# Performance work log

Measured on AMD Instinct MI355X. Metric: run time of the kernel, lower is better.

The kernel has to match this reference:

```python
import jax, jax.numpy as jnp
import numpy as np

N = 4096
IN_DIM = 256
HID = 64
NHEADS = 4
OUT_DIM = 128
ALPHA = 0.5  # LeakyReLU negative slope
NEG_INF = -9e15


def gat_layer(x, mask, W, a, concat):
    """Dense GraphAttentionLayer (pyGAT style).
    x:[N,Fin], mask:[N,N] bool, W:[Fin,Fout], a:[2*Fout]."""
    Wh = x @ W                                   # [N, Fout]
    Fout = W.shape[1]
    f1 = Wh @ a[:Fout]                           # [N]
    f2 = Wh @ a[Fout:]                           # [N]
    e = jax.nn.leaky_relu(f1[:, None] + f2[None, :], negative_slope=ALPHA)  # [N,N]
    att = jax.nn.softmax(jnp.where(mask, e, NEG_INF), axis=1)               # [N,N]
    h = att @ Wh                                 # [N, Fout]
    return jax.nn.elu(h) if concat else h


def setup_inputs() -> dict:
    key = jax.random.key(0)
    ks = jax.random.split(key, 6)
    x = jax.random.normal(ks[0], (N, IN_DIM), dtype=jnp.float32)
    adj = jax.random.randint(ks[1], (N, N), 0, 2, dtype=jnp.int32)
    s_in = 1.0 / np.sqrt(IN_DIM)
    s_hid = 1.0 / np.sqrt(HID * NHEADS)
    W_heads = jax.random.uniform(ks[2], (NHEADS, IN_DIM, HID), jnp.float32, -s_in, s_in)
    a_heads = jax.random.uniform(ks[3], (NHEADS, 2 * HID), jnp.float32, -s_in, s_in)
    W_out = jax.random.uniform(ks[4], (HID * NHEADS, OUT_DIM), jnp.float32, -s_hid, s_hid)
    a_out = jax.random.uniform(ks[5], (2 * OUT_DIM,), jnp.float32, -s_hid, s_hid)
    return {"x": x, "adj": adj, "W_heads": W_heads, "a_heads": a_heads,
            "W_out": W_out, "a_out": a_out}


def reference(x, adj, W_heads, a_heads, W_out, a_out):
    mask = adj > 0
    # multi-head attention, concat along feature dim
    heads = jax.vmap(lambda W, a: gat_layer(x, mask, W, a, True))(W_heads, a_heads)
    h = jnp.transpose(heads, (1, 0, 2)).reshape(N, NHEADS * HID)  # [N, H*HID]
    # dropout=0 -> identity; final GAT layer (concat=False) + outer ELU
    out = jax.nn.elu(gat_layer(h, mask, W_out, a_out, False))     # [N, OUT_DIM]
    return out
```

## Files before the change

kernel.cpp:

```cpp
#include <hip/hip_runtime.h>
#include <hip/hip_bf16.h>

#define N 4096
#define IN_DIM 256
#define HID 64
#define NHEADS 4
#define OUT_DIM 128
#define LOG2E 1.44269504088896340736f

typedef __attribute__((ext_vector_type(8))) short bf16x8;
typedef __attribute__((ext_vector_type(4))) float f32x4;

__global__ __launch_bounds__(256, 4) void prep_kernel(
        const float* __restrict__ x, const float* __restrict__ W,
        const float* __restrict__ a, const int* __restrict__ adj,
        __hip_bfloat16* __restrict__ WhB,
        float* __restrict__ f1, float* __restrict__ f2,
        unsigned* __restrict__ maskT) {
    __shared__ float xs[8 * IN_DIM];
    const int t = threadIdx.x;
    if (blockIdx.x < 512) {
        const int c = t & 63, h = t >> 6;
        const int i0 = blockIdx.x * 8;
        const float4* xg = (const float4*)(x + (size_t)i0 * IN_DIM);
        float4* xs4 = (float4*)xs;
        for (int u = t; u < 8 * IN_DIM / 4; u += 256) xs4[u] = xg[u];
        __syncthreads();
        float acc[8];
#pragma unroll
        for (int r = 0; r < 8; r++) acc[r] = 0.f;
        const float* Wp = W + (size_t)h * IN_DIM * HID + c;
        for (int k = 0; k < IN_DIM; k += 4) {
            const float w0 = Wp[(size_t)(k + 0) * HID];
            const float w1 = Wp[(size_t)(k + 1) * HID];
            const float w2 = Wp[(size_t)(k + 2) * HID];
            const float w3 = Wp[(size_t)(k + 3) * HID];
#pragma unroll
            for (int r = 0; r < 8; r++) {
                const float4 xv = *(const float4*)(xs + r * IN_DIM + k);
                acc[r] += xv.x * w0 + xv.y * w1 + xv.z * w2 + xv.w * w3;
            }
        }
        union { ushort u[8]; uint4 v; } cv;
#pragma unroll
        for (int r = 0; r < 8; r++)
            cv.u[r] = __hip_bfloat16_raw(__float2bfloat16(acc[r])).x;
        const int jblk = i0 >> 5, quad = (i0 >> 3) & 3;
        const int lane_idx = (c & 15) + 16 * quad;
        *(uint4*)(WhB + ((((size_t)h * (N / 32) + jblk) * 4 + (c >> 4)) * 64 +
                         lane_idx) * 8) = cv.v;
        const float av1 = a[h * 2 * HID + c];
        const float av2 = a[h * 2 * HID + HID + c];
        float s1[8], s2[8];
#pragma unroll
        for (int r = 0; r < 8; r++) { s1[r] = acc[r] * av1; s2[r] = acc[r] * av2; }
#pragma unroll
        for (int mm = 32; mm > 0; mm >>= 1) {
#pragma unroll
            for (int r = 0; r < 8; r++) {
                s1[r] += __shfl_xor(s1[r], mm, 64);
                s2[r] += __shfl_xor(s2[r], mm, 64);
            }
        }
        if (c == 0) {
#pragma unroll
            for (int r = 0; r < 8; r++) {
                f1[(size_t)h * N + i0 + r] = s1[r] * LOG2E;
                f2[(size_t)h * N + i0 + r] = s2[r] * LOG2E;
            }
        }
    } else {
        const int lane = t & 63, w = t >> 6;
        const int i = (blockIdx.x - 512) * 4 + w;
        const int4* arow = (const int4*)(adj + (size_t)i * N);
        for (int jb = 0; jb < N / 256; jb++) {
            const int4 a4 = arow[jb * 64 + lane];
            unsigned long long bal[4];
            bal[0] = __ballot(a4.x > 0);
            bal[1] = __ballot(a4.y > 0);
            bal[2] = __ballot(a4.z > 0);
            bal[3] = __ballot(a4.w > 0);
            if (lane < 8) {
                unsigned word = 0;
#pragma unroll
                for (int e = 0; e < 4; e++) {
                    unsigned xv = (unsigned)(bal[e] >> (8 * lane)) & 0xFFu;
                    xv = (xv | (xv << 12)) & 0x000F000Fu;
                    xv = (xv | (xv << 6))  & 0x03030303u;
                    xv = (xv | (xv << 3))  & 0x11111111u;
                    word |= xv << e;
                }
                maskT[(size_t)(jb * 8 + lane) * N + i] = word;
            }
        }
    }
}

template <int HEADS, int D, int DSL, int G, int MW>
__global__ __launch_bounds__(G * 64, 4) void attn_fused(
        const unsigned* __restrict__ maskT,
        const __hip_bfloat16* __restrict__ WhB,
        const float* __restrict__ f1g, const float* __restrict__ f2g,
        float* __restrict__ outp) {
    constexpr int CTtot = D / 16;
    constexpr int CTT = CTtot / DSL;
    constexpr int CC = (D == 64) ? 1 : 2;
    constexpr int KSTEPS = N / (32 * G);
    __shared__ float sh[MW * G * 16 * CC * 17];
    __shared__ float dsh[MW * G * 16];
    const int t = threadIdx.x;
    const int g = t >> 6, lane = t & 63;
    const int m = lane & 15, quad = lane >> 4;
    const int h = blockIdx.y / DSL, slc = blockIdx.y % DSL;
    const int i0 = blockIdx.x * (16 * MW);

    float f1v[MW];
#pragma unroll
    for (int mw = 0; mw < MW; mw++)
        f1v[mw] = f1g[(size_t)h * N + i0 + mw * 16 + m];
    const float* f2p = f2g + (size_t)h * N;
    const bf16x8* whb = (const bf16x8*)WhB + (size_t)h * (N / 32) * CTtot * 64;

    const f32x4 zero = {0.f, 0.f, 0.f, 0.f};
    f32x4 acc[MW][CTT];
    f32x4 sac[MW];
#pragma unroll
    for (int mw = 0; mw < MW; mw++) {
        sac[mw] = zero;
#pragma unroll
        for (int ct = 0; ct < CTT; ct++) acc[mw][ct] = zero;
    }
    const short one_bf = (short)0x3F80;
    const bf16x8 ones = {one_bf, one_bf, one_bf, one_bf,
                         one_bf, one_bf, one_bf, one_bf};

    unsigned mwrd[2][MW];
    float f2v[2][8];
    auto stage_mf = [&](int ks, int b) {
        const int j0 = g * (N / G) + ks * 32;
        const int jw = j0 >> 5;
#pragma unroll
        for (int mw = 0; mw < MW; mw++)
            mwrd[b][mw] = maskT[(size_t)jw * N + i0 + mw * 16 + m];
        const float4 lo = *(const float4*)(f2p + j0 + quad * 8);
        const float4 hi = *(const float4*)(f2p + j0 + quad * 8 + 4);
        f2v[b][0] = lo.x; f2v[b][1] = lo.y; f2v[b][2] = lo.z; f2v[b][3] = lo.w;
        f2v[b][4] = hi.x; f2v[b][5] = hi.y; f2v[b][6] = hi.z; f2v[b][7] = hi.w;
    };

    stage_mf(0, 0);
#pragma unroll 2
    for (int ks = 0; ks < KSTEPS; ks++) {
        const int cur = ks & 1;
        const int jwc = (g * (N / G) + ks * 32) >> 5;
        const bf16x8* bp = whb + ((size_t)jwc * CTtot + slc * CTT) * 64 + lane;
        bf16x8 bfrag[CTT];
#pragma unroll
        for (int ct = 0; ct < CTT; ct++) bfrag[ct] = bp[ct * 64];
        if (ks + 1 < KSTEPS) stage_mf(ks + 1, cur ^ 1);
        bf16x8 afr[MW];
#pragma unroll
        for (int mw = 0; mw < MW; mw++) {
            const unsigned mword = mwrd[cur][mw] >> (quad * 8);
            float p[8];
#pragma unroll
            for (int e = 0; e < 8; e++) {
                const float tt = f1v[mw] + f2v[cur][e];
                const float lr = fmaxf(tt, 0.5f * tt);
                const float pe = __builtin_amdgcn_exp2f(lr);
                p[e] = ((mword >> e) & 1u) ? pe : 0.f;
            }
            union { bf16x8 v; __hip_bfloat162 h2[4]; } u;
#pragma unroll
            for (int e2 = 0; e2 < 4; e2++)
                u.h2[e2] = __float22bfloat162_rn(
                    make_float2(p[2 * e2], p[2 * e2 + 1]));
            afr[mw] = u.v;
        }
#pragma unroll
        for (int ct = 0; ct < CTT; ct++)
#pragma unroll
            for (int mw = 0; mw < MW; mw++)
                acc[mw][ct] = __builtin_amdgcn_mfma_f32_16x16x32_bf16(
                    afr[mw], bfrag[ct], acc[mw][ct], 0, 0, 0);
#pragma unroll
        for (int mw = 0; mw < MW; mw++)
            sac[mw] = __builtin_amdgcn_mfma_f32_16x16x32_bf16(
                afr[mw], ones, sac[mw], 0, 0, 0);
    }

#pragma unroll
    for (int rd = 0; rd < CTT / CC; rd++) {
#pragma unroll
        for (int mw = 0; mw < MW; mw++) {
#pragma unroll
            for (int cc = 0; cc < CC; cc++) {
#pragma unroll
                for (int r = 0; r < 4; r++)
                    sh[(((mw * G + g) * 16 + quad * 4 + r) * CC + cc) * 17 + m] =
                        acc[mw][rd * CC + cc][r];
            }
            if (rd == 0 && m == 0) {
#pragma unroll
                for (int r = 0; r < 4; r++)
                    dsh[(mw * G + g) * 16 + quad * 4 + r] = sac[mw][r];
            }
        }
        __syncthreads();
        if (t < 16 * CC * 16) {
            int row, chl;
            if (D == 64) { row = t & 15; chl = (t >> 4) & 15; }
            else         { chl = t & 31; row = (t >> 5) & 15; }
#pragma unroll
            for (int mw = 0; mw < MW; mw++) {
                float av = 0.f, ss = 0.f;
#pragma unroll
                for (int gg = 0; gg < G; gg++) {
                    av += sh[(((mw * G + gg) * 16 + row) * CC + (chl >> 4)) * 17 +
                             (chl & 15)];
                    ss += dsh[(mw * G + gg) * 16 + row];
                }
                float v = av / ss;
                v = (v > 0.f) ? v : (__builtin_amdgcn_exp2f(v * LOG2E) - 1.f);
                const int chg = h * D + slc * (CTT * 16) + rd * CC * 16 + chl;
                const int irow = i0 + mw * 16 + row;
                if (D == 64)
                    outp[(size_t)chg * N + irow] = v;
                else
                    outp[(size_t)irow * D + chg] = v;
            }
        }
        __syncthreads();
    }
}

__global__ void gemm2_kernel(const float* __restrict__ h1T,
                             const float* __restrict__ W2,
                             const float* __restrict__ a2,
                             __hip_bfloat16* __restrict__ WhB2,
                             float* __restrict__ f1, float* __restrict__ f2) {
    __shared__ float hs[8 * IN_DIM];
    __shared__ float fred[2][2][4][2];
    const int t = threadIdx.x;
    const int c = t & 127, rh = t >> 7;
    const int i0 = blockIdx.x * 8;
    for (int u = t; u < 8 * IN_DIM; u += 256) {
        const int r = u & 7, k = u >> 3;
        hs[r * IN_DIM + k] = h1T[(size_t)k * N + i0 + r];
    }
    __syncthreads();
    float acc[4];
#pragma unroll
    for (int rr = 0; rr < 4; rr++) acc[rr] = 0.f;
    for (int k = 0; k < IN_DIM; k += 4) {
        const float w0 = W2[(size_t)(k + 0) * OUT_DIM + c];
        const float w1 = W2[(size_t)(k + 1) * OUT_DIM + c];
        const float w2 = W2[(size_t)(k + 2) * OUT_DIM + c];
        const float w3 = W2[(size_t)(k + 3) * OUT_DIM + c];
#pragma unroll
        for (int rr = 0; rr < 4; rr++) {
            const float4 hv = *(const float4*)(hs + (rh * 4 + rr) * IN_DIM + k);
            acc[rr] += hv.x * w0 + hv.y * w1 + hv.z * w2 + hv.w * w3;
        }
    }
    union { ushort u[4]; uint2 v; } cv;
#pragma unroll
    for (int rr = 0; rr < 4; rr++)
        cv.u[rr] = __hip_bfloat16_raw(__float2bfloat16(acc[rr])).x;
    const int jblk = i0 >> 5, quad = (i0 >> 3) & 3;
    const int lane_idx = (c & 15) + 16 * quad;
    *(uint2*)((__hip_bfloat16*)WhB2 +
              (((size_t)jblk * 8 + (c >> 4)) * 64 + lane_idx) * 8 + rh * 4) = cv.v;
    const float av1 = a2[c], av2 = a2[OUT_DIM + c];
    float s1[4], s2[4];
#pragma unroll
    for (int rr = 0; rr < 4; rr++) { s1[rr] = acc[rr] * av1; s2[rr] = acc[rr] * av2; }
#pragma unroll
    for (int mm = 32; mm > 0; mm >>= 1) {
#pragma unroll
        for (int rr = 0; rr < 4; rr++) {
            s1[rr] += __shfl_xor(s1[rr], mm, 64);
            s2[rr] += __shfl_xor(s2[rr], mm, 64);
        }
    }
    if ((t & 63) == 0) {
        const int chalf = (t >> 6) & 1;
#pragma unroll
        for (int rr = 0; rr < 4; rr++) {
            fred[rh][chalf][rr][0] = s1[rr];
            fred[rh][chalf][rr][1] = s2[rr];
        }
    }
    __syncthreads();
    if (t < 16) {
        const int fn = t & 1, rr = (t >> 1) & 3, rh2 = t >> 3;
        const float v = (fred[rh2][0][rr][fn] + fred[rh2][1][rr][fn]) * LOG2E;
        (fn ? f2 : f1)[i0 + rh2 * 4 + rr] = v;
    }
}

extern "C" void kernel_launch(void* const* d_in, const int* in_sizes, int n_in,
                              void* d_out, int out_size, void* d_ws, size_t ws_size,
                              hipStream_t stream) {
    const float* x   = (const float*)d_in[0];
    const int*   adj = (const int*)d_in[1];
    const float* Wh_ = (const float*)d_in[2];
    const float* ah  = (const float*)d_in[3];
    const float* W2  = (const float*)d_in[4];
    const float* a2  = (const float*)d_in[5];
    float* out = (float*)d_out;

    float* ws = (float*)d_ws;
    float* f1a = ws;
    float* f2a = f1a + (size_t)NHEADS * N;
    float* f1b = f2a + (size_t)NHEADS * N;
    float* f2b = f1b + N;
    float* h1T = f2b + N;
    __hip_bfloat16* WhB1 = (__hip_bfloat16*)(h1T + (size_t)IN_DIM * N);
    __hip_bfloat16* WhB2 = WhB1 + (size_t)NHEADS * HID * N;
    unsigned* maskT = (unsigned*)(WhB2 + (size_t)OUT_DIM * N);

    prep_kernel<<<1536, 256, 0, stream>>>(x, Wh_, ah, adj, WhB1, f1a, f2a, maskT);
    attn_fused<NHEADS, HID, 1, 8, 2>
        <<<dim3(N / 32, NHEADS), 512, 0, stream>>>(maskT, WhB1, f1a, f2a, h1T);
    gemm2_kernel<<<N / 8, 256, 0, stream>>>(h1T, W2, a2, WhB2, f1b, f2b);
    attn_fused<1, OUT_DIM, 2, 8, 1>
        <<<dim3(N / 16, 2), 512, 0, stream>>>(maskT, WhB2, f1b, f2b, out);
}
```

Measured before the change: 185.7 us.

## Fuse all four stages into one persistent kernel with grid barriers

Merges the prep, first attention, second GEMM and second attention kernels into a single persistent kernel of 512 blocks, separated by atomic-counter grid barriers. This removes three kernel launch boundaries and the idle tails between stages. In exchange it adds a memset launch and spin-wait barriers, and relies on all 512 blocks being co-resident. Work per block also changes: the mask packing and the GEMM2 are redistributed across 512-thread blocks, and the spin loop has a timeout that could silently break correctness.

```diff
diff --git a/kernel.cpp b/kernel.cpp
--- a/kernel.cpp
+++ b/kernel.cpp
@@ -7,112 +7,48 @@
 #define NHEADS 4
 #define OUT_DIM 128
 #define LOG2E 1.44269504088896340736f
+#define NBLK 512
 
 typedef __attribute__((ext_vector_type(8))) short bf16x8;
 typedef __attribute__((ext_vector_type(4))) float f32x4;
 
-__global__ __launch_bounds__(256, 4) void prep_kernel(
-        const float* __restrict__ x, const float* __restrict__ W,
-        const float* __restrict__ a, const int* __restrict__ adj,
-        __hip_bfloat16* __restrict__ WhB,
-        float* __restrict__ f1, float* __restrict__ f2,
-        unsigned* __restrict__ maskT) {
-    __shared__ float xs[8 * IN_DIM];
-    const int t = threadIdx.x;
-    if (blockIdx.x < 512) {
-        const int c = t & 63, h = t >> 6;
-        const int i0 = blockIdx.x * 8;
-        const float4* xg = (const float4*)(x + (size_t)i0 * IN_DIM);
-        float4* xs4 = (float4*)xs;
-        for (int u = t; u < 8 * IN_DIM / 4; u += 256) xs4[u] = xg[u];
-        __syncthreads();
-        float acc[8];
-#pragma unroll
-        for (int r = 0; r < 8; r++) acc[r] = 0.f;
-        const float* Wp = W + (size_t)h * IN_DIM * HID + c;
-        for (int k = 0; k < IN_DIM; k += 4) {
-            const float w0 = Wp[(size_t)(k + 0) * HID];
-            const float w1 = Wp[(size_t)(k + 1) * HID];
-            const float w2 = Wp[(size_t)(k + 2) * HID];
-            const float w3 = Wp[(size_t)(k + 3) * HID];
-#pragma unroll
-            for (int r = 0; r < 8; r++) {
-                const float4 xv = *(const float4*)(xs + r * IN_DIM + k);
-                acc[r] += xv.x * w0 + xv.y * w1 + xv.z * w2 + xv.w * w3;
-            }
-        }
-        union { ushort u[8]; uint4 v; } cv;
-#pragma unroll
-        for (int r = 0; r < 8; r++)
-            cv.u[r] = __hip_bfloat16_raw(__float2bfloat16(acc[r])).x;
-        const int jblk = i0 >> 5, quad = (i0 >> 3) & 3;
-        const int lane_idx = (c & 15) + 16 * quad;
-        *(uint4*)(WhB + ((((size_t)h * (N / 32) + jblk) * 4 + (c >> 4)) * 64 +
-                         lane_idx) * 8) = cv.v;
-        const float av1 = a[h * 2 * HID + c];
-        const float av2 = a[h * 2 * HID + HID + c];
-        float s1[8], s2[8];
-#pragma unroll
-        for (int r = 0; r < 8; r++) { s1[r] = acc[r] * av1; s2[r] = acc[r] * av2; }
-#pragma unroll
-        for (int mm = 32; mm > 0; mm >>= 1) {
-#pragma unroll
-            for (int r = 0; r < 8; r++) {
-                s1[r] += __shfl_xor(s1[r], mm, 64);
-                s2[r] += __shfl_xor(s2[r], mm, 64);
-            }
-        }
-        if (c == 0) {
-#pragma unroll
-            for (int r = 0; r < 8; r++) {
-                f1[(size_t)h * N + i0 + r] = s1[r] * LOG2E;
-                f2[(size_t)h * N + i0 + r] = s2[r] * LOG2E;
-            }
-        }
-    } else {
-        const int lane = t & 63, w = t >> 6;
-        const int i = (blockIdx.x - 512) * 4 + w;
-        const int4* arow = (const int4*)(adj + (size_t)i * N);
-        for (int jb = 0; jb < N / 256; jb++) {
-            const int4 a4 = arow[jb * 64 + lane];
-            unsigned long long bal[4];
-            bal[0] = __ballot(a4.x > 0);
-            bal[1] = __ballot(a4.y > 0);
-            bal[2] = __ballot(a4.z > 0);
-            bal[3] = __ballot(a4.w > 0);
-            if (lane < 8) {
-                unsigned word = 0;
-#pragma unroll
-                for (int e = 0; e < 4; e++) {
-                    unsigned xv = (unsigned)(bal[e] >> (8 * lane)) & 0xFFu;
-                    xv = (xv | (xv << 12)) & 0x000F000Fu;
-                    xv = (xv | (xv << 6))  & 0x03030303u;
-                    xv = (xv | (xv << 3))  & 0x11111111u;
-                    word |= xv << e;
-                }
-                maskT[(size_t)(jb * 8 + lane) * N + i] = word;
-            }
-        }
-    }
+__device__ __forceinline__ void grid_sync(unsigned* cnt) {
+    __syncthreads();
+    if (threadIdx.x == 0) {
+        __threadfence();
+        const unsigned arrived =
+            __hip_atomic_fetch_add(cnt, 1u, __ATOMIC_ACQ_REL,
+                                   __HIP_MEMORY_SCOPE_AGENT) + 1u;
+        if (arrived < NBLK) {
+            int spins = 0;
+            while (__hip_atomic_load(cnt, __ATOMIC_ACQUIRE,
+                                     __HIP_MEMORY_SCOPE_AGENT) < NBLK) {
+                __builtin_amdgcn_s_sleep(1);
+                if (++spins > (1 << 24)) break;
+            }
+        }
+        __threadfence();
+    }
+    __syncthreads();
 }
 
 template <int HEADS, int D, int DSL, int G, int MW>
-__global__ __launch_bounds__(G * 64, 4) void attn_fused(
+__device__ __forceinline__ void attn_stage(
+        const int bx, const int by,
         const unsigned* __restrict__ maskT,
         const __hip_bfloat16* __restrict__ WhB,
         const float* __restrict__ f1g, const float* __restrict__ f2g,
-        float* __restrict__ outp) {
+        float* __restrict__ outp, float* __restrict__ sh,
+        float* __restrict__ dsh) {
     constexpr int CTtot = D / 16;
     constexpr int CTT = CTtot / DSL;
     constexpr int CC = (D == 64) ? 1 : 2;
     constexpr int KSTEPS = N / (32 * G);
-    __shared__ float sh[MW * G * 16 * CC * 17];
-    __shared__ float dsh[MW * G * 16];
     const int t = threadIdx.x;
     const int g = t >> 6, lane = t & 63;
     const int m = lane & 15, quad = lane >> 4;
-    const int h = blockIdx.y / DSL, slc = blockIdx.y % DSL;
-    const int i0 = blockIdx.x * (16 * MW);
+    const int h = by / DSL, slc = by % DSL;
+    const int i0 = bx * (16 * MW);
 
     float f1v[MW];
 #pragma unroll
@@ -234,69 +170,166 @@
     }
 }
 
-__global__ void gemm2_kernel(const float* __restrict__ h1T,
-                             const float* __restrict__ W2,
-                             const float* __restrict__ a2,
-                             __hip_bfloat16* __restrict__ WhB2,
-                             float* __restrict__ f1, float* __restrict__ f2) {
-    __shared__ float hs[8 * IN_DIM];
-    __shared__ float fred[2][2][4][2];
+__global__ __launch_bounds__(512, 4) void mega(
+        const float* __restrict__ x, const float* __restrict__ W,
+        const float* __restrict__ a, const int* __restrict__ adj,
+        const float* __restrict__ W2, const float* __restrict__ a2,
+        __hip_bfloat16* __restrict__ WhB1, __hip_bfloat16* __restrict__ WhB2,
+        float* __restrict__ f1a, float* __restrict__ f2a,
+        float* __restrict__ f1b, float* __restrict__ f2b,
+        float* __restrict__ h1T, unsigned* __restrict__ maskT,
+        float* __restrict__ out, unsigned* __restrict__ bars) {
+    __shared__ float shbuf[4608];
+    __shared__ float dshbuf[256];
     const int t = threadIdx.x;
-    const int c = t & 127, rh = t >> 7;
-    const int i0 = blockIdx.x * 8;
-    for (int u = t; u < 8 * IN_DIM; u += 256) {
-        const int r = u & 7, k = u >> 3;
-        hs[r * IN_DIM + k] = h1T[(size_t)k * N + i0 + r];
-    }
-    __syncthreads();
-    float acc[4];
-#pragma unroll
-    for (int rr = 0; rr < 4; rr++) acc[rr] = 0.f;
-    for (int k = 0; k < IN_DIM; k += 4) {
-        const float w0 = W2[(size_t)(k + 0) * OUT_DIM + c];
-        const float w1 = W2[(size_t)(k + 1) * OUT_DIM + c];
-        const float w2 = W2[(size_t)(k + 2) * OUT_DIM + c];
-        const float w3 = W2[(size_t)(k + 3) * OUT_DIM + c];
-#pragma unroll
-        for (int rr = 0; rr < 4; rr++) {
-            const float4 hv = *(const float4*)(hs + (rh * 4 + rr) * IN_DIM + k);
-            acc[rr] += hv.x * w0 + hv.y * w1 + hv.z * w2 + hv.w * w3;
-        }
-    }
-    union { ushort u[4]; uint2 v; } cv;
-#pragma unroll
-    for (int rr = 0; rr < 4; rr++)
-        cv.u[rr] = __hip_bfloat16_raw(__float2bfloat16(acc[rr])).x;
-    const int jblk = i0 >> 5, quad = (i0 >> 3) & 3;
-    const int lane_idx = (c & 15) + 16 * quad;
-    *(uint2*)((__hip_bfloat16*)WhB2 +
-              (((size_t)jblk * 8 + (c >> 4)) * 64 + lane_idx) * 8 + rh * 4) = cv.v;
-    const float av1 = a2[c], av2 = a2[OUT_DIM + c];
-    float s1[4], s2[4];
-#pragma unroll
-    for (int rr = 0; rr < 4; rr++) { s1[rr] = acc[rr] * av1; s2[rr] = acc[rr] * av2; }
-#pragma unroll
-    for (int mm = 32; mm > 0; mm >>= 1) {
-#pragma unroll
-        for (int rr = 0; rr < 4; rr++) {
-            s1[rr] += __shfl_xor(s1[rr], mm, 64);
-            s2[rr] += __shfl_xor(s2[rr], mm, 64);
-        }
-    }
-    if ((t & 63) == 0) {
-        const int chalf = (t >> 6) & 1;
-#pragma unroll
-        for (int rr = 0; rr < 4; rr++) {
-            fred[rh][chalf][rr][0] = s1[rr];
-            fred[rh][chalf][rr][1] = s2[rr];
-        }
-    }
-    __syncthreads();
-    if (t < 16) {
-        const int fn = t & 1, rr = (t >> 1) & 3, rh2 = t >> 3;
-        const float v = (fred[rh2][0][rr][fn] + fred[rh2][1][rr][fn]) * LOG2E;
-        (fn ? f2 : f1)[i0 + rh2 * 4 + rr] = v;
-    }
+    const int bid = blockIdx.x;
+
+    {
+        const int i0 = bid * 8;
+        float4* xs4 = (float4*)shbuf;
+        const float4* xg = (const float4*)(x + (size_t)i0 * IN_DIM);
+        for (int u = t; u < 8 * IN_DIM / 4; u += 512) xs4[u] = xg[u];
+        __syncthreads();
+        if (t < 256) {
+            const int c = t & 63, h = t >> 6;
+            float acc[8];
+#pragma unroll
+            for (int r = 0; r < 8; r++) acc[r] = 0.f;
+            const float* Wp = W + (size_t)h * IN_DIM * HID + c;
+            for (int k = 0; k < IN_DIM; k += 4) {
+                const float w0 = Wp[(size_t)(k + 0) * HID];
+                const float w1 = Wp[(size_t)(k + 1) * HID];
+                const float w2 = Wp[(size_t)(k + 2) * HID];
+                const float w3 = Wp[(size_t)(k + 3) * HID];
+#pragma unroll
+                for (int r = 0; r < 8; r++) {
+                    const float4 xv = *(const float4*)(shbuf + r * IN_DIM + k);
+                    acc[r] += xv.x * w0 + xv.y * w1 + xv.z * w2 + xv.w * w3;
+                }
+            }
+            union { ushort u[8]; uint4 v; } cv;
+#pragma unroll
+            for (int r = 0; r < 8; r++)
+                cv.u[r] = __hip_bfloat16_raw(__float2bfloat16(acc[r])).x;
+            const int jblk = i0 >> 5, quad = (i0 >> 3) & 3;
+            const int lane_idx = (c & 15) + 16 * quad;
+            *(uint4*)(WhB1 + ((((size_t)h * (N / 32) + jblk) * 4 + (c >> 4)) * 64 +
+                              lane_idx) * 8) = cv.v;
+            const float av1 = a[h * 2 * HID + c];
+            const float av2 = a[h * 2 * HID + HID + c];
+            float s1[8], s2[8];
+#pragma unroll
+            for (int r = 0; r < 8; r++) { s1[r] = acc[r] * av1; s2[r] = acc[r] * av2; }
+#pragma unroll
+            for (int mm = 32; mm > 0; mm >>= 1) {
+#pragma unroll
+                for (int r = 0; r < 8; r++) {
+                    s1[r] += __shfl_xor(s1[r], mm, 64);
+                    s2[r] += __shfl_xor(s2[r], mm, 64);
+                }
+            }
+            if (c == 0) {
+#pragma unroll
+                for (int r = 0; r < 8; r++) {
+                    f1a[(size_t)h * N + i0 + r] = s1[r] * LOG2E;
+                    f2a[(size_t)h * N + i0 + r] = s2[r] * LOG2E;
+                }
+            }
+        } else {
+            const int lane = t & 63, w2 = (t >> 6) - 4;
+            for (int r2 = 0; r2 < 2; r2++) {
+                const int i = i0 + w2 * 2 + r2;
+                const int4* arow = (const int4*)(adj + (size_t)i * N);
+                for (int jb = 0; jb < N / 256; jb++) {
+                    const int4 a4 = arow[jb * 64 + lane];
+                    unsigned long long bal[4];
+                    bal[0] = __ballot(a4.x > 0);
+                    bal[1] = __ballot(a4.y > 0);
+                    bal[2] = __ballot(a4.z > 0);
+                    bal[3] = __ballot(a4.w > 0);
+                    if (lane < 8) {
+                        unsigned word = 0;
+#pragma unroll
+                        for (int e = 0; e < 4; e++) {
+                            unsigned xv = (unsigned)(bal[e] >> (8 * lane)) & 0xFFu;
+                            xv = (xv | (xv << 12)) & 0x000F000Fu;
+                            xv = (xv | (xv << 6))  & 0x03030303u;
+                            xv = (xv | (xv << 3))  & 0x11111111u;
+                            word |= xv << e;
+                        }
+                        maskT[(size_t)(jb * 8 + lane) * N + i] = word;
+                    }
+                }
+            }
+        }
+    }
+    grid_sync(bars + 0);
+
+    attn_stage<NHEADS, HID, 1, 8, 2>(bid & 127, bid >> 7, maskT, WhB1,
+                                     f1a, f2a, h1T, shbuf, dshbuf);
+    grid_sync(bars + 1);
+
+    {
+        float* hs = shbuf;
+        float* fred = dshbuf;
+        const int c = t & 127, rh = t >> 7;
+        const int i0 = bid * 8;
+        for (int u = t; u < 8 * IN_DIM; u += 512) {
+            const int r = u & 7, k = u >> 3;
+            hs[r * IN_DIM + k] = h1T[(size_t)k * N + i0 + r];
+        }
+        __syncthreads();
+        float acc[2] = {0.f, 0.f};
+        for (int k = 0; k < IN_DIM; k += 4) {
+            const float w0 = W2[(size_t)(k + 0) * OUT_DIM + c];
+            const float w1 = W2[(size_t)(k + 1) * OUT_DIM + c];
+            const float w2v = W2[(size_t)(k + 2) * OUT_DIM + c];
+            const float w3 = W2[(size_t)(k + 3) * OUT_DIM + c];
+#pragma unroll
+            for (int rr = 0; rr < 2; rr++) {
+                const float4 hv = *(const float4*)(hs + (rh * 2 + rr) * IN_DIM + k);
+                acc[rr] += hv.x * w0 + hv.y * w1 + hv.z * w2v + hv.w * w3;
+            }
+        }
+        union { ushort u[2]; unsigned v; } cv;
+        cv.u[0] = __hip_bfloat16_raw(__float2bfloat16(acc[0])).x;
+        cv.u[1] = __hip_bfloat16_raw(__float2bfloat16(acc[1])).x;
+        const int jblk = i0 >> 5, quad = (i0 >> 3) & 3;
+        const int lane_idx = (c & 15) + 16 * quad;
+        *(unsigned*)((__hip_bfloat16*)WhB2 +
+                     (((size_t)jblk * 8 + (c >> 4)) * 64 + lane_idx) * 8 + rh * 2) =
+            cv.v;
+        const float av1 = a2[c], av2 = a2[OUT_DIM + c];
+        float s1[2] = {acc[0] * av1, acc[1] * av1};
+        float s2[2] = {acc[0] * av2, acc[1] * av2};
+#pragma unroll
+        for (int mm = 32; mm > 0; mm >>= 1) {
+#pragma unroll
+            for (int rr = 0; rr < 2; rr++) {
+                s1[rr] += __shfl_xor(s1[rr], mm, 64);
+                s2[rr] += __shfl_xor(s2[rr], mm, 64);
+            }
+        }
+        if ((t & 63) == 0) {
+            const int chalf = (t >> 6) & 1;
+#pragma unroll
+            for (int rr = 0; rr < 2; rr++) {
+                fred[((rh * 2 + chalf) * 2 + rr) * 2 + 0] = s1[rr];
+                fred[((rh * 2 + chalf) * 2 + rr) * 2 + 1] = s2[rr];
+            }
+        }
+        __syncthreads();
+        if (t < 16) {
+            const int fn = t & 1, rr = (t >> 1) & 1, rh2 = t >> 2;
+            const float v = (fred[((rh2 * 2 + 0) * 2 + rr) * 2 + fn] +
+                             fred[((rh2 * 2 + 1) * 2 + rr) * 2 + fn]) * LOG2E;
+            (fn ? f2b : f1b)[i0 + rh2 * 2 + rr] = v;
+        }
+    }
+    grid_sync(bars + 2);
+
+    attn_stage<1, OUT_DIM, 2, 8, 1>(bid & 255, bid >> 8, maskT, WhB2,
+                                    f1b, f2b, out, shbuf, dshbuf);
 }
 
 extern "C" void kernel_launch(void* const* d_in, const int* in_sizes, int n_in,
@@ -319,11 +352,9 @@
     __hip_bfloat16* WhB1 = (__hip_bfloat16*)(h1T + (size_t)IN_DIM * N);
     __hip_bfloat16* WhB2 = WhB1 + (size_t)NHEADS * HID * N;
     unsigned* maskT = (unsigned*)(WhB2 + (size_t)OUT_DIM * N);
-
-    prep_kernel<<<1536, 256, 0, stream>>>(x, Wh_, ah, adj, WhB1, f1a, f2a, maskT);
-    attn_fused<NHEADS, HID, 1, 8, 2>
-        <<<dim3(N / 32, NHEADS), 512, 0, stream>>>(maskT, WhB1, f1a, f2a, h1T);
-    gemm2_kernel<<<N / 8, 256, 0, stream>>>(h1T, W2, a2, WhB2, f1b, f2b);
-    attn_fused<1, OUT_DIM, 2, 8, 1>
-        <<<dim3(N / 16, 2), 512, 0, stream>>>(maskT, WhB2, f1b, f2b, out);
+    unsigned* bars = maskT + (size_t)(N / 32) * N;
+
+    hipMemsetAsync(bars, 0, 3 * sizeof(unsigned), stream);
+    mega<<<NBLK, 512, 0, stream>>>(x, Wh_, ah, adj, W2, a2, WhB1, WhB2,
+                                   f1a, f2a, f1b, f2b, h1T, maskT, out, bars);
 }
```

Result: slower. 436.4 us (+135.0%).
